# Kernel optimization log

Hardware: AMD Instinct MI355X
Metric: run time of the kernel (lower is better)

Reference implementation:

```python
import jax, jax.numpy as jnp
import numpy as np

B, S, D = 4, 2048, 1024
H, DK, DV = 16, 64, 64


def setup_inputs() -> dict:
    key = jax.random.key(0)
    kx, kq, kk, kv, ko = jax.random.split(key, 5)
    scale = 0.02
    return {
        "x": jax.random.normal(kx, (B, S, D), dtype=jnp.float32),
        "Wq": jax.random.normal(kq, (H, D, DK), dtype=jnp.float32) * scale,
        "Wk": jax.random.normal(kk, (H, D, DK), dtype=jnp.float32) * scale,
        "Wv": jax.random.normal(kv, (H, D, DV), dtype=jnp.float32) * scale,
        "Wo": jax.random.normal(ko, (H * DV, D), dtype=jnp.float32) * scale,
    }


def reference(x, Wq, Wk, Wv, Wo):
    # Per-head projections, batched over heads with einsum (same math as
    # the original per-head Linear loop).
    q = jnp.einsum("bsd,hdk->bhsk", x, Wq)  # [B,H,S,DK]
    k = jnp.einsum("bsd,hdk->bhsk", x, Wk)  # [B,H,S,DK]
    v = jnp.einsum("bsd,hdv->bhsv", x, Wv)  # [B,H,S,DV]

    scores = jnp.einsum("bhqk,bhsk->bhqs", q, k) / jnp.sqrt(
        jnp.asarray(DK, dtype=x.dtype)
    )  # [B,H,S,S]
    # Causal mask: position q attends only to s <= q.
    causal = jnp.tril(jnp.ones((S, S), dtype=bool))
    scores = jnp.where(causal, scores, jnp.asarray(-1e9, dtype=scores.dtype))
    attn = jax.nn.softmax(scores, axis=-1)

    ctx = jnp.einsum("bhqs,bhsv->bhqv", attn, v)  # [B,H,S,DV]
    # Concat heads: [B,S,H*DV], then output projection (no bias).
    ctx = ctx.transpose(0, 2, 1, 3).reshape(B, S, H * DV)
    return ctx @ Wo  # [B,S,D]
```

## Files before the change

kernel.cpp:

```cpp
#include <hip/hip_runtime.h>
#include <hip/hip_bf16.h>

#define SB 2048
#define DM 1024
#define NH 16
#define HD 64
#define BB 4
#define MTOT (BB * SB)
#define NW (DM * DM)

typedef __attribute__((ext_vector_type(8))) short bf16x8;
typedef __attribute__((ext_vector_type(4))) short bf16x4;
typedef __attribute__((ext_vector_type(4))) float f32x4;
typedef __attribute__((ext_vector_type(4))) __fp16 f16x4;
typedef __attribute__((ext_vector_type(2))) __fp16 f16x2;

__device__ __forceinline__ short f2bf(float f) {
    union { float f; unsigned u; } a; a.f = f;
    unsigned r = (a.u + 0x7FFF + ((a.u >> 16) & 1)) >> 16;
    return (short)r;
}

__global__ __launch_bounds__(256) void cvt_x(const float* __restrict__ in,
                                             short* __restrict__ out) {
    const int i = (blockIdx.x * 256 + threadIdx.x) * 8;
    float4 v0 = *(const float4*)(in + i);
    float4 v1 = *(const float4*)(in + i + 4);
    bf16x8 o = { f2bf(v0.x), f2bf(v0.y), f2bf(v0.z), f2bf(v0.w),
                 f2bf(v1.x), f2bf(v1.y), f2bf(v1.z), f2bf(v1.w) };
    *(bf16x8*)(out + i) = o;
}

__global__ __launch_bounds__(256) void cvt_w4(const float* __restrict__ Wq,
                                              const float* __restrict__ Wk,
                                              const float* __restrict__ Wv,
                                              const float* __restrict__ Wo,
                                              short* __restrict__ wall,
                                              short* __restrict__ wot) {
    __shared__ float Ls[64][65];
    const int bid = blockIdx.x;
    const int which = bid >> 8;
    const int rem = bid & 255;
    const float* in;
    short* out;
    int R, C;
    if (which < 3) {
        in = (which == 0) ? Wq : (which == 1) ? Wk : Wv;
        out = wall + (size_t)which * NW;
        R = DM; C = HD;
    } else {
        in = Wo; out = wot; R = DM; C = DM;
    }
    const int tilesC = C >> 6, tilesR = R >> 6;
    const int b = rem / (tilesR * tilesC);
    const int rem2 = rem % (tilesR * tilesC);
    const int R0 = (rem2 / tilesC) << 6;
    const int C0 = (rem2 % tilesC) << 6;
    const float* src = in + (size_t)b * R * C;
    short* dst = out + (size_t)b * R * C;
    const int t = threadIdx.x;
    const int r = t >> 2, c4 = (t & 3) << 4;
    const float* p = src + (size_t)(R0 + r) * C + C0 + c4;
#pragma unroll
    for (int u = 0; u < 16; u += 4) {
        float4 v = *(const float4*)(p + u);
        Ls[r][c4 + u] = v.x; Ls[r][c4 + u + 1] = v.y;
        Ls[r][c4 + u + 2] = v.z; Ls[r][c4 + u + 3] = v.w;
    }
    __syncthreads();
    const int cc = t >> 2, u2 = (t & 3) << 4;
    short* q = dst + (size_t)(C0 + cc) * R + R0 + u2;
    bf16x8 o0, o1;
#pragma unroll
    for (int j = 0; j < 8; ++j) o0[j] = f2bf(Ls[u2 + j][cc]);
#pragma unroll
    for (int j = 0; j < 8; ++j) o1[j] = f2bf(Ls[u2 + 8 + j][cc]);
    *(bf16x8*)(q) = o0;
    *(bf16x8*)(q + 8) = o1;
}

__global__ __launch_bounds__(256) void mm_qkv(const short* __restrict__ A,
                                              const short* __restrict__ BT,
                                              short* __restrict__ qO,
                                              short* __restrict__ kO,
                                              _Float16* __restrict__ vO) {
    __shared__ short sA[128 * 32];
    __shared__ short sB[128 * 32];
    const int t = threadIdx.x;
    const int lane = t & 63;
    const int w = t >> 6;
    const int wm = w >> 1, wn = w & 1;
    const int l15 = lane & 15, quad = lane >> 4;
    const int m0 = blockIdx.x * 128;
    const int n0 = blockIdx.y * 128;
    const bool isV = (n0 >= 2048);

    f32x4 acc[4][4] = {};
    const int row0 = t >> 2;
    const int kc = (t & 3) * 8;

    for (int k0 = 0; k0 < DM; k0 += 32) {
#pragma unroll
        for (int u = 0; u < 2; ++u) {
            const short* ga = A + (size_t)(m0 + u * 64 + row0) * DM + k0 + kc;
            const short* gb = BT + (size_t)(n0 + u * 64 + row0) * DM + k0 + kc;
            __builtin_amdgcn_global_load_lds(
                (const __attribute__((address_space(1))) unsigned*)ga,
                (__attribute__((address_space(3))) unsigned*)&sA[(u * 64 + row0) * 32 + kc],
                16, 0, 0);
            __builtin_amdgcn_global_load_lds(
                (const __attribute__((address_space(1))) unsigned*)gb,
                (__attribute__((address_space(3))) unsigned*)&sB[(u * 64 + row0) * 32 + kc],
                16, 0, 0);
        }
        __syncthreads();

        bf16x8 af[4], bfr[4];
#pragma unroll
        for (int i = 0; i < 4; ++i) {
            af[i]  = *(const bf16x8*)&sA[(wm * 64 + i * 16 + l15) * 32 + quad * 8];
            bfr[i] = *(const bf16x8*)&sB[(wn * 64 + i * 16 + l15) * 32 + quad * 8];
        }
        if (isV) {
#pragma unroll
            for (int i = 0; i < 4; ++i)
#pragma unroll
                for (int j = 0; j < 4; ++j)
                    acc[i][j] = __builtin_amdgcn_mfma_f32_16x16x32_bf16(af[i], bfr[j],
                                                                        acc[i][j], 0, 0, 0);
        } else {
#pragma unroll
            for (int i = 0; i < 4; ++i)
#pragma unroll
                for (int j = 0; j < 4; ++j)
                    acc[i][j] = __builtin_amdgcn_mfma_f32_16x16x32_bf16(bfr[j], af[i],
                                                                        acc[i][j], 0, 0, 0);
        }
        __syncthreads();
    }

    if (isV) {
#pragma unroll
        for (int i = 0; i < 4; ++i) {
            const int m = m0 + wm * 64 + i * 16 + quad * 4;
            const int b = m >> 11, s0 = m & (SB - 1);
#pragma unroll
            for (int j = 0; j < 4; ++j) {
                const int nv = (n0 - 2048) + wn * 64 + j * 16 + l15;
                const int h = nv >> 6, d = nv & 63;
                f16x2 a = __builtin_amdgcn_cvt_pkrtz(acc[i][j][0], acc[i][j][1]);
                f16x2 b2 = __builtin_amdgcn_cvt_pkrtz(acc[i][j][2], acc[i][j][3]);
                f16x4 o = {a.x, a.y, b2.x, b2.y};
                *(f16x4*)&vO[((size_t)((b * NH + h) * HD + d)) * SB + s0] = o;
            }
        }
    } else {
#pragma unroll
        for (int i = 0; i < 4; ++i) {
            const int m = m0 + wm * 64 + i * 16 + l15;
            const int b = m >> 11, s = m & (SB - 1);
#pragma unroll
            for (int j = 0; j < 4; ++j) {
                const int n = n0 + wn * 64 + j * 16 + quad * 4;
                const int seg = n >> 10;
                const int h = (n & 1023) >> 6, d0 = n & 63;
                const float sc = (seg == 0) ? 0.125f : 1.0f;
                bf16x4 o;
#pragma unroll
                for (int r = 0; r < 4; ++r) o[r] = f2bf(acc[i][j][r] * sc);
                short* dst = (seg == 0) ? qO : kO;
                *(bf16x4*)&dst[(((size_t)(b * NH + h) * SB + s) << 6) + d0] = o;
            }
        }
    }
}

__global__ __launch_bounds__(256) void mm_out(const short* __restrict__ A,
                                              const short* __restrict__ BT,
                                              float* __restrict__ fO) {
    __shared__ short sA[128 * 32];
    __shared__ short sB[128 * 32];
    const int t = threadIdx.x;
    const int lane = t & 63;
    const int w = t >> 6;
    const int wm = w >> 1, wn = w & 1;
    const int l15 = lane & 15, quad = lane >> 4;
    const int m0 = blockIdx.x * 128;
    const int n0 = blockIdx.y * 128;

    f32x4 acc[4][4] = {};
    const int row0 = t >> 2;
    const int kc = (t & 3) * 8;

    for (int k0 = 0; k0 < DM; k0 += 32) {
#pragma unroll
        for (int u = 0; u < 2; ++u) {
            const short* ga = A + (size_t)(m0 + u * 64 + row0) * DM + k0 + kc;
            const short* gb = BT + (size_t)(n0 + u * 64 + row0) * DM + k0 + kc;
            __builtin_amdgcn_global_load_lds(
                (const __attribute__((address_space(1))) unsigned*)ga,
                (__attribute__((address_space(3))) unsigned*)&sA[(u * 64 + row0) * 32 + kc],
                16, 0, 0);
            __builtin_amdgcn_global_load_lds(
                (const __attribute__((address_space(1))) unsigned*)gb,
                (__attribute__((address_space(3))) unsigned*)&sB[(u * 64 + row0) * 32 + kc],
                16, 0, 0);
        }
        __syncthreads();

        bf16x8 af[4], bfr[4];
#pragma unroll
        for (int i = 0; i < 4; ++i) {
            af[i]  = *(const bf16x8*)&sA[(wm * 64 + i * 16 + l15) * 32 + quad * 8];
            bfr[i] = *(const bf16x8*)&sB[(wn * 64 + i * 16 + l15) * 32 + quad * 8];
        }
#pragma unroll
        for (int i = 0; i < 4; ++i)
#pragma unroll
            for (int j = 0; j < 4; ++j)
                acc[i][j] = __builtin_amdgcn_mfma_f32_16x16x32_bf16(bfr[j], af[i],
                                                                    acc[i][j], 0, 0, 0);
        __syncthreads();
    }

#pragma unroll
    for (int i = 0; i < 4; ++i) {
        const int m = m0 + wm * 64 + i * 16 + l15;
#pragma unroll
        for (int j = 0; j < 4; ++j) {
            const int n = n0 + wn * 64 + j * 16 + quad * 4;
            f32x4 v = acc[i][j];
            *(float4*)&fO[(size_t)m * DM + n] = *(float4*)&v;
        }
    }
}

__global__ __launch_bounds__(256) void attn_mfma(const short* __restrict__ Q,
                                                 const short* __restrict__ K,
                                                 const _Float16* __restrict__ VT,
                                                 short* __restrict__ ctx) {
    __shared__ short    sK[2][64 * 64];
    __shared__ _Float16 sV[2][64 * 64];

    const int t = threadIdx.x;
    const int lane = t & 63, w = t >> 6;
    const int l15 = lane & 15, quad = lane >> 4;
    const int idx = blockIdx.x;
    const int bh = ((idx >> 7) << 3) | (idx & 7);
    const int pair = (idx >> 3) & 15;
    const int b = bh >> 4, h = bh & 15;
    const size_t hb = (size_t)bh * SB * HD;
    const short* Qb = Q + hb;
    const short* Kb = K + hb;
    const _Float16* Vb = VT + hb;

    const int srow = t >> 3;
    const int sch  = t & 7;
    const int srow2 = srow + 32;
    const int swl = l15 & 7;

    auto stage = [&](int k0, int bbuf) {
        __builtin_amdgcn_global_load_lds(
            (const __attribute__((address_space(1))) unsigned*)
                (Kb + (size_t)(k0 + srow) * HD + ((sch ^ (srow & 7)) << 3)),
            (__attribute__((address_space(3))) unsigned*)&sK[bbuf][t << 3], 16, 0, 0);
        __builtin_amdgcn_global_load_lds(
            (const __attribute__((address_space(1))) unsigned*)
                (Kb + (size_t)(k0 + srow2) * HD + ((sch ^ (srow2 & 7)) << 3)),
            (__attribute__((address_space(3))) unsigned*)&sK[bbuf][(t + 256) << 3], 16, 0, 0);
        __builtin_amdgcn_global_load_lds(
            (const __attribute__((address_space(1))) unsigned*)
                (Vb + (size_t)srow * SB + k0 + ((sch ^ (srow & 7)) << 3)),
            (__attribute__((address_space(3))) unsigned*)&sV[bbuf][t << 3], 16, 0, 0);
        __builtin_amdgcn_global_load_lds(
            (const __attribute__((address_space(1))) unsigned*)
                (Vb + (size_t)srow2 * SB + k0 + ((sch ^ (srow2 & 7)) << 3)),
            (__attribute__((address_space(3))) unsigned*)&sV[bbuf][(t + 256) << 3], 16, 0, 0);
    };

#pragma unroll
    for (int ph = 0; ph < 2; ++ph) {
        const int qt = ph ? (31 - pair) : pair;
        const int qw = qt * 64 + w * 16;

        bf16x8 aq[2];
#pragma unroll
        for (int hh = 0; hh < 2; ++hh)
            aq[hh] = *(const bf16x8*)(Qb + (size_t)(qw + l15) * HD + hh * 32 + quad * 8);

        f32x4 O[4] = {};
        float l_r = 0.f;

        __syncthreads();
        stage(0, 0);

        for (int kt = 0; kt <= qt; ++kt) {
            __syncthreads();
            if (kt < qt) stage((kt + 1) * 64, (kt + 1) & 1);

            const int buf = kt & 1;
            const bool diag = (kt == qt);
            const short* sKb = &sK[buf][0];
            const _Float16* sVb = &sV[buf][0];

            f32x4 sc[4] = {};
#pragma unroll
            for (int st = 0; st < 4; ++st) {
                const int row = st * 16 + l15;
#pragma unroll
                for (int hh = 0; hh < 2; ++hh) {
                    bf16x8 kf = *(const bf16x8*)&sKb[(row << 6) +
                                                     (((hh * 4 + quad) ^ swl) << 3)];
                    sc[st] = __builtin_amdgcn_mfma_f32_16x16x32_bf16(kf, aq[hh], sc[st], 0, 0, 0);
                }
            }

#pragma unroll
            for (int st = 0; st < 4; ++st) {
                if (diag && st > w) break;
                f16x4 vf[4];
                const int vch = ((st * 2 + (quad >> 1)) ^ swl) << 3;
#pragma unroll
                for (int dj = 0; dj < 4; ++dj)
                    vf[dj] = *(const f16x4*)&sVb[((dj * 16 + l15) << 6) + vch + (quad & 1) * 4];
                float p[4];
                if (!diag || st < w) {
#pragma unroll
                    for (int r = 0; r < 4; ++r) p[r] = __expf(sc[st][r]);
                } else {
#pragma unroll
                    for (int r = 0; r < 4; ++r)
                        p[r] = (quad * 4 + r <= l15) ? __expf(sc[st][r]) : 0.f;
                }
                l_r += (p[0] + p[1]) + (p[2] + p[3]);
                f16x2 pa = __builtin_amdgcn_cvt_pkrtz(p[0], p[1]);
                f16x2 pb = __builtin_amdgcn_cvt_pkrtz(p[2], p[3]);
                f16x4 pf = {pa.x, pa.y, pb.x, pb.y};
#pragma unroll
                for (int dj = 0; dj < 4; ++dj)
                    O[dj] = __builtin_amdgcn_mfma_f32_16x16x16f16(vf[dj], pf, O[dj], 0, 0, 0);
            }
        }

        float l = l_r;
        l += __shfl_xor(l, 16);
        l += __shfl_xor(l, 32);
        const float inv = 1.f / l;
        const int q = qw + l15;
#pragma unroll
        for (int dj = 0; dj < 4; ++dj) {
            bf16x4 o;
#pragma unroll
            for (int r = 0; r < 4; ++r) o[r] = f2bf(O[dj][r] * inv);
            *(bf16x4*)&ctx[(size_t)(b * SB + q) * DM + h * HD + dj * 16 + quad * 4] = o;
        }
    }
}

extern "C" void kernel_launch(void* const* d_in, const int* in_sizes, int n_in,
                              void* d_out, int out_size, void* d_ws, size_t ws_size,
                              hipStream_t stream) {
    const float* x  = (const float*)d_in[0];
    const float* Wq = (const float*)d_in[1];
    const float* Wk = (const float*)d_in[2];
    const float* Wv = (const float*)d_in[3];
    const float* Wo = (const float*)d_in[4];
    float* out = (float*)d_out;

    const size_t NX = (size_t)MTOT * DM;
    short* xb   = (short*)d_ws;
    short* wall = xb + NX;
    short* wot  = wall + 3 * (size_t)NW;
    short* qb   = wot + NW;
    short* kb   = qb + NX;
    short* vtb  = kb + NX;
    short* ctxb = vtb + NX;

    dim3 blk(256);
    cvt_x<<<NX / (256 * 8), blk, 0, stream>>>(x, xb);
    cvt_w4<<<1024, blk, 0, stream>>>(Wq, Wk, Wv, Wo, wall, wot);

    dim3 gqkv(MTOT / 128, 3072 / 128);
    mm_qkv<<<gqkv, blk, 0, stream>>>(xb, wall, qb, kb, (_Float16*)vtb);

    attn_mfma<<<dim3(1024), blk, 0, stream>>>(qb, kb, (const _Float16*)vtb, ctxb);

    dim3 gout(MTOT / 128, DM / 128);
    mm_out<<<gout, blk, 0, stream>>>(ctxb, wot, out);
}
```

Before: 263.2 us.

## Merge conversion kernels, deepen GEMM K-tile with swizzled LDS, use exp2 softmax

Fuses the x and weight conversion kernels into one launch, and replaces both GEMM kernels with a templated version that stages a K-depth of 64 instead of 32. LDS reads use an XOR-swizzled layout to avoid bank conflicts. The Q scale now folds in log2(e) so attention can call the hardware exp2 directly, and the attention key loop is unrolled by 2. This cuts per-tile barriers, launch overhead and exp cost, at the price of twice the LDS per block, which may lower occupancy.

```diff
diff --git a/kernel.cpp b/kernel.cpp
--- a/kernel.cpp
+++ b/kernel.cpp
@@ -8,6 +8,7 @@
 #define BB 4
 #define MTOT (BB * SB)
 #define NW (DM * DM)
+#define QSCALE 0.1803368801111244f
 
 typedef __attribute__((ext_vector_type(8))) short bf16x8;
 typedef __attribute__((ext_vector_type(4))) short bf16x4;
@@ -21,26 +22,29 @@
     return (short)r;
 }
 
-__global__ __launch_bounds__(256) void cvt_x(const float* __restrict__ in,
-                                             short* __restrict__ out) {
-    const int i = (blockIdx.x * 256 + threadIdx.x) * 8;
-    float4 v0 = *(const float4*)(in + i);
-    float4 v1 = *(const float4*)(in + i + 4);
-    bf16x8 o = { f2bf(v0.x), f2bf(v0.y), f2bf(v0.z), f2bf(v0.w),
-                 f2bf(v1.x), f2bf(v1.y), f2bf(v1.z), f2bf(v1.w) };
-    *(bf16x8*)(out + i) = o;
-}
-
-__global__ __launch_bounds__(256) void cvt_w4(const float* __restrict__ Wq,
-                                              const float* __restrict__ Wk,
-                                              const float* __restrict__ Wv,
-                                              const float* __restrict__ Wo,
-                                              short* __restrict__ wall,
-                                              short* __restrict__ wot) {
+__global__ __launch_bounds__(256) void cvt_all(const float* __restrict__ x,
+                                               const float* __restrict__ Wq,
+                                               const float* __restrict__ Wk,
+                                               const float* __restrict__ Wv,
+                                               const float* __restrict__ Wo,
+                                               short* __restrict__ xb,
+                                               short* __restrict__ wall,
+                                               short* __restrict__ wot) {
+    const int bid = blockIdx.x;
+    const int t = threadIdx.x;
+    if (bid < 4096) {
+        const int i = (bid * 256 + t) * 8;
+        float4 v0 = *(const float4*)(x + i);
+        float4 v1 = *(const float4*)(x + i + 4);
+        bf16x8 o = { f2bf(v0.x), f2bf(v0.y), f2bf(v0.z), f2bf(v0.w),
+                     f2bf(v1.x), f2bf(v1.y), f2bf(v1.z), f2bf(v1.w) };
+        *(bf16x8*)(xb + i) = o;
+        return;
+    }
     __shared__ float Ls[64][65];
-    const int bid = blockIdx.x;
-    const int which = bid >> 8;
-    const int rem = bid & 255;
+    const int rem = bid - 4096;
+    const int which = rem >> 8;
+    const int rem2 = rem & 255;
     const float* in;
     short* out;
     int R, C;
@@ -52,13 +56,12 @@
         in = Wo; out = wot; R = DM; C = DM;
     }
     const int tilesC = C >> 6, tilesR = R >> 6;
-    const int b = rem / (tilesR * tilesC);
-    const int rem2 = rem % (tilesR * tilesC);
-    const int R0 = (rem2 / tilesC) << 6;
-    const int C0 = (rem2 % tilesC) << 6;
+    const int b = rem2 / (tilesR * tilesC);
+    const int rr = rem2 % (tilesR * tilesC);
+    const int R0 = (rr / tilesC) << 6;
+    const int C0 = (rr % tilesC) << 6;
     const float* src = in + (size_t)b * R * C;
     short* dst = out + (size_t)b * R * C;
-    const int t = threadIdx.x;
     const int r = t >> 2, c4 = (t & 3) << 4;
     const float* p = src + (size_t)(R0 + r) * C + C0 + c4;
 #pragma unroll
@@ -79,13 +82,15 @@
     *(bf16x8*)(q + 8) = o1;
 }
 
-__global__ __launch_bounds__(256) void mm_qkv(const short* __restrict__ A,
-                                              const short* __restrict__ BT,
-                                              short* __restrict__ qO,
-                                              short* __restrict__ kO,
-                                              _Float16* __restrict__ vO) {
-    __shared__ short sA[128 * 32];
-    __shared__ short sB[128 * 32];
+template <int MODE>
+__global__ __launch_bounds__(256) void mm64(const short* __restrict__ A,
+                                            const short* __restrict__ BT,
+                                            short* __restrict__ qO,
+                                            short* __restrict__ kO,
+                                            _Float16* __restrict__ vO,
+                                            float* __restrict__ fO) {
+    __shared__ short sA[128 * 64];
+    __shared__ short sB[128 * 64];
     const int t = threadIdx.x;
     const int lane = t & 63;
     const int w = t >> 6;
@@ -93,53 +98,74 @@
     const int l15 = lane & 15, quad = lane >> 4;
     const int m0 = blockIdx.x * 128;
     const int n0 = blockIdx.y * 128;
-    const bool isV = (n0 >= 2048);
+    const bool isV = (MODE == 0) && (n0 >= 2048);
 
     f32x4 acc[4][4] = {};
-    const int row0 = t >> 2;
-    const int kc = (t & 3) * 8;
-
-    for (int k0 = 0; k0 < DM; k0 += 32) {
-#pragma unroll
-        for (int u = 0; u < 2; ++u) {
-            const short* ga = A + (size_t)(m0 + u * 64 + row0) * DM + k0 + kc;
-            const short* gb = BT + (size_t)(n0 + u * 64 + row0) * DM + k0 + kc;
+    const int srow = t >> 3;
+    const int schunk = t & 7;
+    const int ssrc = ((schunk ^ (srow & 7)) << 3);
+    const int sdst = (schunk << 3);
+    const int r7 = l15 & 7;
+
+    for (int k0 = 0; k0 < DM; k0 += 64) {
+#pragma unroll
+        for (int u = 0; u < 4; ++u) {
+            const int row = u * 32 + srow;
+            const short* ga = A + (size_t)(m0 + row) * DM + k0 + ssrc;
+            const short* gb = BT + (size_t)(n0 + row) * DM + k0 + ssrc;
             __builtin_amdgcn_global_load_lds(
                 (const __attribute__((address_space(1))) unsigned*)ga,
-                (__attribute__((address_space(3))) unsigned*)&sA[(u * 64 + row0) * 32 + kc],
+                (__attribute__((address_space(3))) unsigned*)&sA[(row << 6) + sdst],
                 16, 0, 0);
             __builtin_amdgcn_global_load_lds(
                 (const __attribute__((address_space(1))) unsigned*)gb,
-                (__attribute__((address_space(3))) unsigned*)&sB[(u * 64 + row0) * 32 + kc],
+                (__attribute__((address_space(3))) unsigned*)&sB[(row << 6) + sdst],
                 16, 0, 0);
         }
         __syncthreads();
 
-        bf16x8 af[4], bfr[4];
+#pragma unroll
+        for (int half = 0; half < 2; ++half) {
+            bf16x8 af[4], bfr[4];
+#pragma unroll
+            for (int i = 0; i < 4; ++i) {
+                const int ra = wm * 64 + i * 16 + l15;
+                const int rb = wn * 64 + i * 16 + l15;
+                const int ch = ((half * 4 + quad) ^ r7) << 3;
+                af[i]  = *(const bf16x8*)&sA[(ra << 6) + ch];
+                bfr[i] = *(const bf16x8*)&sB[(rb << 6) + ch];
+            }
+            if (isV) {
+#pragma unroll
+                for (int i = 0; i < 4; ++i)
+#pragma unroll
+                    for (int j = 0; j < 4; ++j)
+                        acc[i][j] = __builtin_amdgcn_mfma_f32_16x16x32_bf16(af[i], bfr[j],
+                                                                            acc[i][j], 0, 0, 0);
+            } else {
+#pragma unroll
+                for (int i = 0; i < 4; ++i)
+#pragma unroll
+                    for (int j = 0; j < 4; ++j)
+                        acc[i][j] = __builtin_amdgcn_mfma_f32_16x16x32_bf16(bfr[j], af[i],
+                                                                            acc[i][j], 0, 0, 0);
+            }
+        }
+        __syncthreads();
+    }
+
+    if (MODE == 1) {
 #pragma unroll
         for (int i = 0; i < 4; ++i) {
-            af[i]  = *(const bf16x8*)&sA[(wm * 64 + i * 16 + l15) * 32 + quad * 8];
-            bfr[i] = *(const bf16x8*)&sB[(wn * 64 + i * 16 + l15) * 32 + quad * 8];
-        }
-        if (isV) {
-#pragma unroll
-            for (int i = 0; i < 4; ++i)
-#pragma unroll
-                for (int j = 0; j < 4; ++j)
-                    acc[i][j] = __builtin_amdgcn_mfma_f32_16x16x32_bf16(af[i], bfr[j],
-                                                                        acc[i][j], 0, 0, 0);
-        } else {
-#pragma unroll
-            for (int i = 0; i < 4; ++i)
-#pragma unroll
-                for (int j = 0; j < 4; ++j)
-                    acc[i][j] = __builtin_amdgcn_mfma_f32_16x16x32_bf16(bfr[j], af[i],
-                                                                        acc[i][j], 0, 0, 0);
-        }
-        __syncthreads();
-    }
-
-    if (isV) {
+            const int m = m0 + wm * 64 + i * 16 + l15;
+#pragma unroll
+            for (int j = 0; j < 4; ++j) {
+                const int n = n0 + wn * 64 + j * 16 + quad * 4;
+                f32x4 v = acc[i][j];
+                *(float4*)&fO[(size_t)m * DM + n] = *(float4*)&v;
+            }
+        }
+    } else if (isV) {
 #pragma unroll
         for (int i = 0; i < 4; ++i) {
             const int m = m0 + wm * 64 + i * 16 + quad * 4;
@@ -164,73 +190,13 @@
                 const int n = n0 + wn * 64 + j * 16 + quad * 4;
                 const int seg = n >> 10;
                 const int h = (n & 1023) >> 6, d0 = n & 63;
-                const float sc = (seg == 0) ? 0.125f : 1.0f;
+                const float sc = (seg == 0) ? QSCALE : 1.0f;
                 bf16x4 o;
 #pragma unroll
                 for (int r = 0; r < 4; ++r) o[r] = f2bf(acc[i][j][r] * sc);
                 short* dst = (seg == 0) ? qO : kO;
                 *(bf16x4*)&dst[(((size_t)(b * NH + h) * SB + s) << 6) + d0] = o;
             }
-        }
-    }
-}
-
-__global__ __launch_bounds__(256) void mm_out(const short* __restrict__ A,
-                                              const short* __restrict__ BT,
-                                              float* __restrict__ fO) {
-    __shared__ short sA[128 * 32];
-    __shared__ short sB[128 * 32];
-    const int t = threadIdx.x;
-    const int lane = t & 63;
-    const int w = t >> 6;
-    const int wm = w >> 1, wn = w & 1;
-    const int l15 = lane & 15, quad = lane >> 4;
-    const int m0 = blockIdx.x * 128;
-    const int n0 = blockIdx.y * 128;
-
-    f32x4 acc[4][4] = {};
-    const int row0 = t >> 2;
-    const int kc = (t & 3) * 8;
-
-    for (int k0 = 0; k0 < DM; k0 += 32) {
-#pragma unroll
-        for (int u = 0; u < 2; ++u) {
-            const short* ga = A + (size_t)(m0 + u * 64 + row0) * DM + k0 + kc;
-            const short* gb = BT + (size_t)(n0 + u * 64 + row0) * DM + k0 + kc;
-            __builtin_amdgcn_global_load_lds(
-                (const __attribute__((address_space(1))) unsigned*)ga,
-                (__attribute__((address_space(3))) unsigned*)&sA[(u * 64 + row0) * 32 + kc],
-                16, 0, 0);
-            __builtin_amdgcn_global_load_lds(
-                (const __attribute__((address_space(1))) unsigned*)gb,
-                (__attribute__((address_space(3))) unsigned*)&sB[(u * 64 + row0) * 32 + kc],
-                16, 0, 0);
-        }
-        __syncthreads();
-
-        bf16x8 af[4], bfr[4];
-#pragma unroll
-        for (int i = 0; i < 4; ++i) {
-            af[i]  = *(const bf16x8*)&sA[(wm * 64 + i * 16 + l15) * 32 + quad * 8];
-            bfr[i] = *(const bf16x8*)&sB[(wn * 64 + i * 16 + l15) * 32 + quad * 8];
-        }
-#pragma unroll
-        for (int i = 0; i < 4; ++i)
-#pragma unroll
-            for (int j = 0; j < 4; ++j)
-                acc[i][j] = __builtin_amdgcn_mfma_f32_16x16x32_bf16(bfr[j], af[i],
-                                                                    acc[i][j], 0, 0, 0);
-        __syncthreads();
-    }
-
-#pragma unroll
-    for (int i = 0; i < 4; ++i) {
-        const int m = m0 + wm * 64 + i * 16 + l15;
-#pragma unroll
-        for (int j = 0; j < 4; ++j) {
-            const int n = n0 + wn * 64 + j * 16 + quad * 4;
-            f32x4 v = acc[i][j];
-            *(float4*)&fO[(size_t)m * DM + n] = *(float4*)&v;
         }
     }
 }
@@ -294,6 +260,7 @@
         __syncthreads();
         stage(0, 0);
 
+#pragma unroll 2
         for (int kt = 0; kt <= qt; ++kt) {
             __syncthreads();
             if (kt < qt) stage((kt + 1) * 64, (kt + 1) & 1);
@@ -326,11 +293,11 @@
                 float p[4];
                 if (!diag || st < w) {
 #pragma unroll
-                    for (int r = 0; r < 4; ++r) p[r] = __expf(sc[st][r]);
+                    for (int r = 0; r < 4; ++r) p[r] = __builtin_amdgcn_exp2f(sc[st][r]);
                 } else {
 #pragma unroll
                     for (int r = 0; r < 4; ++r)
-                        p[r] = (quad * 4 + r <= l15) ? __expf(sc[st][r]) : 0.f;
+                        p[r] = (quad * 4 + r <= l15) ? __builtin_amdgcn_exp2f(sc[st][r]) : 0.f;
                 }
                 l_r += (p[0] + p[1]) + (p[2] + p[3]);
                 f16x2 pa = __builtin_amdgcn_cvt_pkrtz(p[0], p[1]);
@@ -377,14 +344,13 @@
     short* ctxb = vtb + NX;
 
     dim3 blk(256);
-    cvt_x<<<NX / (256 * 8), blk, 0, stream>>>(x, xb);
-    cvt_w4<<<1024, blk, 0, stream>>>(Wq, Wk, Wv, Wo, wall, wot);
+    cvt_all<<<4096 + 1024, blk, 0, stream>>>(x, Wq, Wk, Wv, Wo, xb, wall, wot);
 
     dim3 gqkv(MTOT / 128, 3072 / 128);
-    mm_qkv<<<gqkv, blk, 0, stream>>>(xb, wall, qb, kb, (_Float16*)vtb);
+    mm64<0><<<gqkv, blk, 0, stream>>>(xb, wall, qb, kb, (_Float16*)vtb, nullptr);
 
     attn_mfma<<<dim3(1024), blk, 0, stream>>>(qb, kb, (const _Float16*)vtb, ctxb);
 
     dim3 gout(MTOT / 128, DM / 128);
-    mm_out<<<gout, blk, 0, stream>>>(ctxb, wot, out);
-}
+    mm64<1><<<gout, blk, 0, stream>>>(ctxb, wot, nullptr, nullptr, nullptr, out);
+}
```

Measured after the change: 242.5 us. 1.09x faster.
